# Performance work log

Hardware: AMD Instinct MI355X
Metric: run time of the kernel (lower is better)

## Reference

```python
import jax, jax.numpy as jnp
import numpy as np

N_EMBED = 1024
N_HEAD = 16
HEAD_SIZE = N_EMBED // N_HEAD  # 64
SEQ = 2048
BATCH = 2
EPS = 1e-5


def setup_inputs() -> dict:
    key = jax.random.key(0)
    ks = jax.random.split(key, 16)
    s = lambda fan_in: 1.0 / np.sqrt(fan_in)
    d, h, hs, f = N_EMBED, N_HEAD, HEAD_SIZE, 4 * N_EMBED
    return {
        "x": jax.random.normal(ks[0], (BATCH, SEQ, d), dtype=jnp.float32),
        # per-head QKV projections (no bias), stacked over heads: [H, D, hs]
        "wq": jax.random.normal(ks[1], (h, d, hs), dtype=jnp.float32) * s(d),
        "wk": jax.random.normal(ks[2], (h, d, hs), dtype=jnp.float32) * s(d),
        "wv": jax.random.normal(ks[3], (h, d, hs), dtype=jnp.float32) * s(d),
        "w_proj": jax.random.normal(ks[4], (d, d), dtype=jnp.float32) * s(d),
        "b_proj": jnp.zeros((d,), dtype=jnp.float32),
        "w1": jax.random.normal(ks[5], (d, f), dtype=jnp.float32) * s(d),
        "b1": jnp.zeros((f,), dtype=jnp.float32),
        "w2": jax.random.normal(ks[6], (f, d), dtype=jnp.float32) * s(f),
        "b2": jnp.zeros((d,), dtype=jnp.float32),
        "g1": jnp.ones((d,), dtype=jnp.float32),
        "be1": jnp.zeros((d,), dtype=jnp.float32),
        "g2": jnp.ones((d,), dtype=jnp.float32),
        "be2": jnp.zeros((d,), dtype=jnp.float32),
    }


def _layer_norm(x, gamma, beta):
    mu = jnp.mean(x, axis=-1, keepdims=True)
    var = jnp.mean(jnp.square(x - mu), axis=-1, keepdims=True)
    return (x - mu) * jax.lax.rsqrt(var + EPS) * gamma + beta


def reference(x, wq, wk, wv, w_proj, b_proj, w1, b1, w2, b2, g1, be1, g2, be2):
    B, S, D = x.shape
    # per-head projections (vectorized over heads): [B, H, S, hs]
    q = jnp.einsum("bsd,hdk->bhsk", x, wq)
    k = jnp.einsum("bsd,hdk->bhsk", x, wk)
    v = jnp.einsum("bsd,hdk->bhsk", x, wv)
    scale = HEAD_SIZE ** -0.5
    scores = jnp.einsum("bhsk,bhtk->bhst", q, k) * scale  # [B,H,S,S]
    causal = jnp.tril(jnp.ones((S, S), dtype=bool))
    scores = jnp.where(causal, scores, -jnp.inf)
    w = jax.nn.softmax(scores, axis=-1)  # dropout=0 -> identity
    attn = jnp.einsum("bhst,bhtk->bhsk", w, v)  # [B,H,S,hs]
    # concat heads (head-major ordering matches torch.cat over heads)
    attn = attn.transpose(0, 2, 1, 3).reshape(B, S, D)
    y = attn @ w_proj + b_proj
    x = _layer_norm(x + y, g1, be1)
    y = jax.nn.relu(x @ w1 + b1) @ w2 + b2
    x = _layer_norm(x + y, g2, be2)
    return x
```

## Files before the change

kernel.cpp:

```cpp
#include <hip/hip_runtime.h>


typedef unsigned short u16;
typedef unsigned int u32;
typedef __attribute__((ext_vector_type(8))) short bf16x8;
typedef __attribute__((ext_vector_type(4))) float f32x4;
typedef __attribute__((ext_vector_type(2))) u32 u32x2;
typedef __attribute__((ext_vector_type(4))) _Float16 f16x4;

#define MFMA16(a, b, c) __builtin_amdgcn_mfma_f32_16x16x32_bf16(a, b, c, 0, 0, 0)
#define MFMAH(a, b, c) __builtin_amdgcn_mfma_f32_16x16x16f16(a, b, c, 0, 0, 0)

__device__ __forceinline__ u16 f2b(float f) {
  unsigned int u = __builtin_bit_cast(unsigned int, f);
  u = (u + 0x7fffu + ((u >> 16) & 1u)) >> 16;
  return (u16)u;
}

__device__ __forceinline__ void gload_lds16(const u16* g, u16* l) {
  __builtin_amdgcn_global_load_lds((const __attribute__((address_space(1))) void*)g,
                                   (__attribute__((address_space(3))) void*)l, 16, 0, 0);
}

__device__ __forceinline__ u32 pkrtz(float lo, float hi) {
  return __builtin_bit_cast(u32, __builtin_amdgcn_cvt_pkrtz(lo, hi));
}

__device__ __forceinline__ f16x4 pack4h(float a, float b, float c, float d) {
  u32x2 r = {pkrtz(a, b), pkrtz(c, d)};
  return __builtin_bit_cast(f16x4, r);
}

__device__ __forceinline__ u16 f2h(float v) {
  return __builtin_bit_cast(u16, (_Float16)v);
}


__global__ __launch_bounds__(256) void pack_all(
    const float* __restrict__ x, const float* __restrict__ wq,
    const float* __restrict__ wk, const float* __restrict__ wv,
    const float* __restrict__ wp, const float* __restrict__ w1,
    const float* __restrict__ w2, u16* __restrict__ Xbf, u16* __restrict__ WqkvT,
    u16* __restrict__ WprojT, u16* __restrict__ W1T, u16* __restrict__ W2T) {
  int bid = blockIdx.x;
  int t = threadIdx.x;
  if (bid >= 12288) {
    size_t i = ((size_t)(bid - 12288) * 256 + t) * 4;
    float4 v = *(const float4*)(x + i);
    Xbf[i + 0] = f2b(v.x);
    Xbf[i + 1] = f2b(v.y);
    Xbf[i + 2] = f2b(v.z);
    Xbf[i + 3] = f2b(v.w);
    return;
  }
  __shared__ float tile[32][33];
  int tx = t & 31, ty = t >> 5;
  const float* src;
  u16* dst;
  int R, C, r0, c0;
  float scale = 1.0f;
  if (bid < 3072) {
    int z = bid >> 6, q = bid & 63;
    int p = z >> 4, h = z & 15;
    src = (p == 0 ? wq : (p == 1 ? wk : wv)) + (size_t)h * 1024 * 64;
    scale = (p == 0) ? 0.1803368801f : 1.0f;
    dst = WqkvT + (size_t)(p * 1024 + h * 64) * 1024;
    R = 1024; C = 64;
    c0 = (q & 1) * 32; r0 = (q >> 1) * 32;
  } else if (bid < 4096) {
    int q = bid - 3072;
    src = wp; dst = WprojT; R = 1024; C = 1024;
    c0 = (q & 31) * 32; r0 = (q >> 5) * 32;
  } else if (bid < 8192) {
    int q = bid - 4096;
    src = w1; dst = W1T; R = 1024; C = 4096;
    c0 = (q & 127) * 32; r0 = (q >> 7) * 32;
  } else {
    int q = bid - 8192;
    src = w2; dst = W2T; R = 4096; C = 1024;
    c0 = (q & 31) * 32; r0 = (q >> 5) * 32;
  }
#pragma unroll
  for (int i = 0; i < 4; ++i)
    tile[ty + i * 8][tx] = src[(size_t)(r0 + ty + i * 8) * C + c0 + tx];
  __syncthreads();
#pragma unroll
  for (int i = 0; i < 4; ++i)
    dst[(size_t)(c0 + ty + i * 8) * R + r0 + tx] = f2b(tile[tx][ty + i * 8] * scale);
}


template <int MODE>
__global__ __launch_bounds__(256, 4) void gemm_bf16(const u16* __restrict__ A,
                                                    const u16* __restrict__ Bt, int M,
                                                    int N, int Kc, int lda,
                                                    const float* __restrict__ bias,
                                                    u16* __restrict__ outB, int ldc,
                                                    u16* __restrict__ vtg) {
  constexpr int BM = 128, BN = 128, BK = 64;
  constexpr int IM = 4, JN = 4;
  __shared__ u16 As[BM * BK];
  __shared__ u16 Bs[BN * BK];
  int t = threadIdx.x;
  int m0 = blockIdx.x * BM, n0 = blockIdx.y * BN;
  int kb = blockIdx.z * Kc;
  int lane = t & 63, wid = t >> 6;
  int wm = (wid >> 1) * 64, wn = (wid & 1) * 64;
  int m16 = lane & 15, quad = lane >> 4;
  int sw = m16 & 7;

  f32x4 acc[IM][JN] = {};

  for (int k0 = kb; k0 < kb + Kc; k0 += BK) {
    __syncthreads();
#pragma unroll
    for (int i = 0; i < 4; ++i) {
      int S = i * 256 + t;
      int row = S >> 3, c = S & 7;
      gload_lds16(&A[(size_t)(m0 + row) * lda + k0 + (c ^ (row & 7)) * 8],
                  &As[(i * 256 + wid * 64) * 8]);
    }
#pragma unroll
    for (int i = 0; i < 4; ++i) {
      int S = i * 256 + t;
      int row = S >> 3, c = S & 7;
      gload_lds16(&Bt[(size_t)(n0 + row) * lda + k0 + (c ^ (row & 7)) * 8],
                  &Bs[(i * 256 + wid * 64) * 8]);
    }
    __syncthreads();
#pragma unroll
    for (int kk = 0; kk < 2; ++kk) {
      bf16x8 af[IM], bfr[JN];
      int slot = (kk * 4 + quad) ^ sw;
#pragma unroll
      for (int i = 0; i < IM; ++i)
        af[i] = *(const bf16x8*)&As[(wm + i * 16 + m16) * BK + slot * 8];
#pragma unroll
      for (int j = 0; j < JN; ++j)
        bfr[j] = *(const bf16x8*)&Bs[(wn + j * 16 + m16) * BK + slot * 8];
#pragma unroll
      for (int i = 0; i < IM; ++i)
#pragma unroll
        for (int j = 0; j < JN; ++j) acc[i][j] = MFMA16(af[i], bfr[j], acc[i][j]);
    }
  }

  if (MODE == 3 && n0 >= 2048) {
#pragma unroll
    for (int i = 0; i < IM; ++i)
#pragma unroll
      for (int j = 0; j < JN; ++j) {
        int dg = n0 + wn + j * 16 + m16 - 2048;
        int hh = dg >> 6, dd = dg & 63;
        int token = m0 + wm + i * 16 + quad * 4;
        int bb = token >> 11, tt = token & 2047;
        u32x2 pv = {pkrtz(acc[i][j][0], acc[i][j][1]),
                    pkrtz(acc[i][j][2], acc[i][j][3])};
        *(u32x2*)&vtg[(((size_t)bb * 16 + hh) * 64 + dd) * 2048 + tt] = pv;
      }
    return;
  }

  u16* pb = (MODE == 4) ? outB + (size_t)blockIdx.z * M * N : outB;
#pragma unroll
  for (int i = 0; i < IM; ++i)
#pragma unroll
    for (int j = 0; j < JN; ++j) {
      int col = n0 + wn + j * 16 + m16;
      float bv = (MODE == 1) ? bias[col] : 0.0f;
#pragma unroll
      for (int r = 0; r < 4; ++r) {
        int row = m0 + wm + i * 16 + quad * 4 + r;
        float v = acc[i][j][r];
        if (MODE == 1) {
          v += bv;
          v = v > 0.0f ? v : 0.0f;
          pb[(size_t)row * ldc + col] = f2b(v);
        } else if (MODE == 4) {
          pb[(size_t)row * ldc + col] = f2h(v);
        } else {
          pb[(size_t)row * ldc + col] = f2b(v);
        }
      }
    }
}


__constant__ unsigned char R_QB[40] = {
    15, 15, 15, 15, 14, 14, 11, 11, 11, 10, 7,  7,  3,
    14, 14, 13, 13, 13, 13, 12, 12, 10, 10, 9,  9,  6,  6,
    12, 12, 9,  8,  8,  8,  5,  5,  2,
    4,  4,  1,  0};
__constant__ unsigned char R_K0[40] = {
    0,  8,  16, 24, 0,  8,  0,  8,  16, 0,  0,  8,  0,
    16, 23, 0,  7,  14, 21, 0,  7,  8,  15, 0,  7,  0,  7,
    14, 20, 14, 0,  6,  12, 0,  6,  0,
    0,  5,  0,  0};
__constant__ unsigned char R_NIT[40] = {
    8, 8, 8, 8, 8, 8, 8, 8, 8, 8, 8, 8, 8,
    7, 7, 7, 7, 7, 7, 7, 7, 7, 7, 7, 7, 7, 7,
    6, 6, 6, 6, 6, 6, 6, 6, 6,
    5, 5, 4, 2};
__constant__ unsigned char R_ST[40] = {
    32, 33, 34, 35, 28, 29, 17, 18, 19, 14, 6,  7,  255,
    30, 31, 24, 25, 26, 27, 20, 21, 15, 16, 11, 12, 4,  5,
    22, 23, 13, 8,  9,  10, 2,  3,  255,
    0,  1,  255, 255};
__constant__ unsigned char CB_BASE[12] = {0, 2, 4, 6, 8, 11, 14, 17, 20, 24, 28, 32};

__global__ __launch_bounds__(256) void attn_part(const u16* __restrict__ qk,
                                                 const u16* __restrict__ vtg,
                                                 u16* __restrict__ attn_out,
                                                 u16* __restrict__ opart0,
                                                 u16* __restrict__ opart1,
                                                 float2* __restrict__ ml) {
  int rank = blockIdx.x >> 5, bh = blockIdx.x & 31;
  int qb = R_QB[rank];
  int k_start = R_K0[rank] * 64;
  int iters = R_NIT[rank];
  int st = R_ST[rank];
  int b = bh >> 4, h = bh & 15;

  int t = threadIdx.x, lane = t & 63, w = t >> 6;
  int m16 = lane & 15, quad = lane >> 4;
  int wq0 = qb * 128 + w * 32;

  __shared__ u16 Ks[2][64 * 64];
  __shared__ u16 Vs[2][64 * 64];

  bf16x8 qa[2][2];
#pragma unroll
  for (int qs = 0; qs < 2; ++qs) {
    const u16* qp = qk + (size_t)(b * 2048 + wq0 + qs * 16 + m16) * 2048 + h * 64;
    qa[qs][0] = *(const bf16x8*)&qp[quad * 8];
    qa[qs][1] = *(const bf16x8*)&qp[32 + quad * 8];
  }

  f32x4 oT[2][4] = {};
  f32x4 oL[2] = {};
  const f16x4 ones = {(_Float16)1.0f, (_Float16)1.0f, (_Float16)1.0f, (_Float16)1.0f};

  int row0 = t >> 3, c0 = t & 7;
  int row1 = 32 + row0;
  const u16* kbase = qk + (size_t)(b * 2048) * 2048 + 1024 + h * 64;
  const u16* vbase = vtg + ((size_t)(b * 16 + h) * 64) * 2048;
  int sw = m16 & 7;

#define STAGE_ASYNC(T0, BUF)                                                        \
  {                                                                                 \
    gload_lds16(&kbase[(size_t)((T0) + row0) * 2048 + (c0 ^ (row0 & 7)) * 8],       \
                &Ks[BUF][(w * 64) * 8]);                                            \
    gload_lds16(&kbase[(size_t)((T0) + row1) * 2048 + (c0 ^ (row1 & 7)) * 8],       \
                &Ks[BUF][(256 + w * 64) * 8]);                                      \
    gload_lds16(&vbase[(size_t)row0 * 2048 + (T0) + (c0 ^ (row0 & 7)) * 8],         \
                &Vs[BUF][(w * 64) * 8]);                                            \
    gload_lds16(&vbase[(size_t)row1 * 2048 + (T0) + (c0 ^ (row1 & 7)) * 8],         \
                &Vs[BUF][(256 + w * 64) * 8]);                                      \
  }

  STAGE_ASYNC(k_start, 0);
  __syncthreads();

  for (int it = 0; it < iters; ++it) {
    int t0 = k_start + it * 64;
    int cur = it & 1;
    if (it + 1 < iters) STAGE_ASYNC(t0 + 64, !cur);

    if (t0 <= wq0 + 31) {
      f32x4 sv[2][4];
      __builtin_amdgcn_s_setprio(1);
#pragma unroll
      for (int ts = 0; ts < 4; ++ts) {
        bf16x8 ka0 = *(const bf16x8*)&Ks[cur][(ts * 16 + m16) * 64 + (quad ^ sw) * 8];
        bf16x8 ka1 =
            *(const bf16x8*)&Ks[cur][(ts * 16 + m16) * 64 + ((4 + quad) ^ sw) * 8];
#pragma unroll
        for (int qs = 0; qs < 2; ++qs) {
          f32x4 a = {};
          a = MFMA16(ka0, qa[qs][0], a);
          a = MFMA16(ka1, qa[qs][1], a);
          sv[qs][ts] = a;
        }
      }
      __builtin_amdgcn_s_setprio(0);
      if (t0 + 63 > wq0) {
#pragma unroll
        for (int qs = 0; qs < 2; ++qs)
#pragma unroll
          for (int ts = 0; ts < 4; ++ts)
#pragma unroll
            for (int rr = 0; rr < 4; ++rr) {
              int key = t0 + ts * 16 + quad * 4 + rr;
              if (key > wq0 + qs * 16 + m16) sv[qs][ts][rr] = -3e38f;
            }
      }
      f16x4 pf[2][4];
#pragma unroll
      for (int qs = 0; qs < 2; ++qs)
#pragma unroll
        for (int ts = 0; ts < 4; ++ts) {
          float p0 = exp2f(sv[qs][ts][0] - 8.0f);
          float p1 = exp2f(sv[qs][ts][1] - 8.0f);
          float p2 = exp2f(sv[qs][ts][2] - 8.0f);
          float p3 = exp2f(sv[qs][ts][3] - 8.0f);
          pf[qs][ts] = pack4h(p0, p1, p2, p3);
        }
      __builtin_amdgcn_s_setprio(1);
#pragma unroll
      for (int ts = 0; ts < 4; ++ts) {
        oL[0] = MFMAH(ones, pf[0][ts], oL[0]);
        oL[1] = MFMAH(ones, pf[1][ts], oL[1]);
#pragma unroll
        for (int ds = 0; ds < 4; ++ds) {
          f16x4 av = __builtin_bit_cast(
              f16x4, *(const u32x2*)&Vs[cur][(ds * 16 + m16) * 64 +
                                             (((ts * 2 + (quad >> 1)) ^ sw) * 8) +
                                             (quad & 1) * 4]);
          oT[0][ds] = MFMAH(av, pf[0][ts], oT[0][ds]);
          oT[1][ds] = MFMAH(av, pf[1][ts], oT[1][ds]);
        }
      }
      __builtin_amdgcn_s_setprio(0);
    }
    __syncthreads();
  }
#undef STAGE_ASYNC

  if (st == 255) {
#pragma unroll
    for (int qs = 0; qs < 2; ++qs) {
      float rl = 1.0f / oL[qs][0];
      int q = wq0 + qs * 16 + m16;
#pragma unroll
      for (int ds = 0; ds < 4; ++ds) {
        f32x4 o = oT[qs][ds];
        u32x2 ov = {(u32)f2b(o[0] * rl) | ((u32)f2b(o[1] * rl) << 16),
                    (u32)f2b(o[2] * rl) | ((u32)f2b(o[3] * rl) << 16)};
        *(u32x2*)&attn_out[(size_t)(b * 2048 + q) * 1024 + h * 64 + ds * 16 +
                           quad * 4] = ov;
      }
    }
  } else {
    u16* po;
    size_t sb;
    if (st < 32) {
      po = opart0;
      sb = ((size_t)st * 32 + bh) * 128;
    } else {
      po = opart1;
      sb = ((size_t)(st - 32) * 32 + bh) * 128;
    }
    size_t mlb = ((size_t)st * 32 + bh) * 128;
#pragma unroll
    for (int qs = 0; qs < 2; ++qs) {
      float ls = oL[qs][0];
      int qloc = w * 32 + qs * 16 + m16;
#pragma unroll
      for (int ds = 0; ds < 4; ++ds) {
        f32x4 o = oT[qs][ds];
        u32x2 ov = {pkrtz(o[0], o[1]), pkrtz(o[2], o[3])};
        *(u32x2*)&po[(sb + qloc) * 64 + ds * 16 + quad * 4] = ov;
      }
      if (quad == 0) ml[mlb + qloc] = make_float2(0.0f, ls);
    }
  }
}

__global__ __launch_bounds__(256) void attn_comb(const u16* __restrict__ opart0,
                                                 const u16* __restrict__ opart1,
                                                 const float2* __restrict__ ml,
                                                 u16* __restrict__ attn_out) {
  int qb = 4 + blockIdx.x, bh = blockIdx.y;
  int b = bh >> 4, h = bh & 15;
  int nseg = (qb < 8) ? 2 : (qb < 12 ? 3 : 4);
  int base = CB_BASE[qb - 4];
  int t = threadIdx.x;
  int q = t >> 1, dh = (t & 1) * 32;

  float lsum = 0.0f;
  for (int s = 0; s < nseg; ++s)
    lsum += ml[((size_t)(base + s) * 32 + bh) * 128 + q].y;
  float rl = 1.0f / lsum;

  constexpr size_t SLOT = (size_t)32 * 128 * 64;
  const u16* orow[4];
  for (int s = 0; s < nseg; ++s) {
    int sa = base + s;
    const u16* bp =
        (sa < 32) ? opart0 + (size_t)sa * SLOT : opart1 + (size_t)(sa - 32) * SLOT;
    orow[s] = bp + ((size_t)bh * 128 + q) * 64 + dh;
  }

  size_t oout = (size_t)(b * 2048 + qb * 128 + q) * 1024 + h * 64 + dh;
#pragma unroll 2
  for (int dd = 0; dd < 32; dd += 4) {
    float o0 = 0, o1 = 0, o2 = 0, o3 = 0;
    for (int s = 0; s < nseg; ++s) {
      f16x4 hv = __builtin_bit_cast(f16x4, *(const u32x2*)&orow[s][dd]);
      o0 += (float)hv[0];
      o1 += (float)hv[1];
      o2 += (float)hv[2];
      o3 += (float)hv[3];
    }
    u32x2 ov = {(u32)f2b(o0 * rl) | ((u32)f2b(o1 * rl) << 16),
                (u32)f2b(o2 * rl) | ((u32)f2b(o3 * rl) << 16)};
    *(u32x2*)&attn_out[oout + dd] = ov;
  }
}


__global__ __launch_bounds__(256) void ln_comb(const u16* __restrict__ parts, int np,
                                               const float* __restrict__ bias,
                                               const float* __restrict__ resid,
                                               const float* __restrict__ g,
                                               const float* __restrict__ be,
                                               float* __restrict__ outF,
                                               u16* __restrict__ outB) {
  int row = blockIdx.x;
  int t = threadIdx.x;
  size_t off = (size_t)row * 1024 + t * 4;
  float4 bv4 = *(const float4*)(bias + t * 4);
  float a0 = bv4.x, a1 = bv4.y, a2 = bv4.z, a3 = bv4.w;
  for (int c = 0; c < np; ++c) {
    f16x4 hv =
        __builtin_bit_cast(f16x4, *(const u32x2*)&parts[(size_t)c * 4096 * 1024 + off]);
    a0 += (float)hv[0];
    a1 += (float)hv[1];
    a2 += (float)hv[2];
    a3 += (float)hv[3];
  }
  float4 rv = *(const float4*)(resid + off);
  a0 += rv.x;
  a1 += rv.y;
  a2 += rv.z;
  a3 += rv.w;

  float s = a0 + a1 + a2 + a3;
  float sq = a0 * a0 + a1 * a1 + a2 * a2 + a3 * a3;
#pragma unroll
  for (int d = 1; d < 64; d <<= 1) {
    s += __shfl_xor(s, d);
    sq += __shfl_xor(sq, d);
  }
  __shared__ float red[8];
  int lane = t & 63, wid = t >> 6;
  if (lane == 0) {
    red[wid] = s;
    red[4 + wid] = sq;
  }
  __syncthreads();
  s = red[0] + red[1] + red[2] + red[3];
  sq = red[4] + red[5] + red[6] + red[7];
  float mu = s * (1.0f / 1024.0f);
  float var = sq * (1.0f / 1024.0f) - mu * mu;
  float rstd = rsqrtf(var + 1e-5f);
  float4 gv = *(const float4*)(g + t * 4);
  float4 bev = *(const float4*)(be + t * 4);
  float o0 = (a0 - mu) * rstd * gv.x + bev.x;
  float o1 = (a1 - mu) * rstd * gv.y + bev.y;
  float o2 = (a2 - mu) * rstd * gv.z + bev.z;
  float o3 = (a3 - mu) * rstd * gv.w + bev.w;
  if (outF) {
    float4 ov = {o0, o1, o2, o3};
    *(float4*)(outF + off) = ov;
  }
  if (outB) {
    outB[off + 0] = f2b(o0);
    outB[off + 1] = f2b(o1);
    outB[off + 2] = f2b(o2);
    outB[off + 3] = f2b(o3);
  }
}


extern "C" void kernel_launch(void* const* d_in, const int* in_sizes, int n_in,
                              void* d_out, int out_size, void* d_ws, size_t ws_size,
                              hipStream_t stream) {
  const float* x = (const float*)d_in[0];
  const float* wq = (const float*)d_in[1];
  const float* wk = (const float*)d_in[2];
  const float* wv = (const float*)d_in[3];
  const float* w_proj = (const float*)d_in[4];
  const float* b_proj = (const float*)d_in[5];
  const float* w1 = (const float*)d_in[6];
  const float* b1 = (const float*)d_in[7];
  const float* w2 = (const float*)d_in[8];
  const float* b2 = (const float*)d_in[9];
  const float* g1 = (const float*)d_in[10];
  const float* be1 = (const float*)d_in[11];
  const float* g2 = (const float*)d_in[12];
  const float* be2 = (const float*)d_in[13];
  float* out = (float*)d_out;

  const int M = 4096;
  char* w = (char*)d_ws;
  u16* Xbf = (u16*)w;        w += (size_t)M * 1024 * 2;
  u16* WqkvT = (u16*)w;      w += (size_t)3072 * 1024 * 2;
  u16* WprojT = (u16*)w;     w += (size_t)1024 * 1024 * 2;
  u16* W1T = (u16*)w;        w += (size_t)4096 * 1024 * 2;
  u16* X1b = (u16*)w;        w += (size_t)M * 1024 * 2;
  u16* W2T = (u16*)w;        w += (size_t)1024 * 4096 * 2;
  u16* QK = (u16*)w;         w += (size_t)M * 2048 * 2;
  u16* Vtg = (u16*)w;        w += (size_t)2 * 16 * 64 * 2048 * 2;
  u16* Attn = (u16*)w;       w += (size_t)M * 1024 * 2;
  float* X1f = (float*)w;    w += (size_t)M * 1024 * 4;

  u16* Pdown = Xbf;
  u16* Pproj = QK;
  u16* Hbuf = QK;
  u16* Opart0 = (u16*)X1f;
  u16* Opart1 = Xbf;
  float2* Ml = (float2*)((char*)d_ws + (size_t)4 * 1024 * 1024);

  pack_all<<<16384, 256, 0, stream>>>(x, wq, wk, wv, w_proj, w1, w2, Xbf, WqkvT,
                                      WprojT, W1T, W2T);

  gemm_bf16<3><<<dim3(32, 24, 1), 256, 0, stream>>>(Xbf, WqkvT, M, 3072, 1024, 1024,
                                                    nullptr, QK, 2048, Vtg);

  attn_part<<<1280, 256, 0, stream>>>(QK, Vtg, Attn, Opart0, Opart1, Ml);
  attn_comb<<<dim3(12, 32), 256, 0, stream>>>(Opart0, Opart1, Ml, Attn);

  gemm_bf16<4><<<dim3(32, 8, 2), 256, 0, stream>>>(Attn, WprojT, M, 1024, 512, 1024,
                                                   nullptr, Pproj, 1024, nullptr);
  ln_comb<<<M, 256, 0, stream>>>(Pproj, 2, b_proj, x, g1, be1, X1f, X1b);

  gemm_bf16<1><<<dim3(32, 32, 1), 256, 0, stream>>>(X1b, W1T, M, 4096, 1024, 1024, b1,
                                                    Hbuf, 4096, nullptr);

  gemm_bf16<4><<<dim3(32, 8, 4), 256, 0, stream>>>(Hbuf, W2T, M, 1024, 1024, 4096,
                                                   nullptr, Pdown, 1024, nullptr);
  ln_comb<<<M, 256, 0, stream>>>(Pdown, 4, b2, X1f, g2, be2, out, nullptr);
}
```

Measured before the change: 330.9 us.

## Add 256x256-tile 8-wave GEMM kernel for the FFN up-projection

New measurement: 365.1 us. +10.3%, slower.

```diff
diff --git a/kernel.cpp b/kernel.cpp
--- a/kernel.cpp
+++ b/kernel.cpp
@@ -186,6 +186,180 @@
 }
 
 
+template <int MODE>
+__global__ __launch_bounds__(512) void gemm8(const u16* __restrict__ A,
+                                             const u16* __restrict__ Bt, int M, int N,
+                                             int Kc, int lda,
+                                             const float* __restrict__ bias,
+                                             u16* __restrict__ outB, int ldc) {
+  __shared__ __align__(16) u16 As[2][2][128 * 64];
+  __shared__ __align__(16) u16 Bs[2][2][128 * 64];
+  int t = threadIdx.x;
+  int lane = t & 63, wid = t >> 6;
+  int m16 = lane & 15, quad = lane >> 4, sw = m16 & 7;
+  int wr = wid >> 2, wc = wid & 3;
+  int m0 = blockIdx.x * 256, n0 = blockIdx.y * 256;
+  int kb = blockIdx.z * Kc;
+  int NT = Kc >> 6;
+
+  int ahalf = t >> 8;
+  int at = t & 255;
+  int aw = wid & 3;
+  int brow0 = (wc & 1) * 64;
+
+  f32x4 acc[8][4] = {};
+  bf16x8 afc[2][2], afn[2][2], bfc[4][2], bfn[4][2];
+
+#define STAGE_B(bf, bh, kt)                                                        \
+  {                                                                                \
+    _Pragma("unroll") for (int l = 0; l < 2; ++l) {                                \
+      int slot = l * 512 + t;                                                      \
+      int row = slot >> 3, c = slot & 7;                                           \
+      gload_lds16(&Bt[(size_t)(n0 + (bh)*128 + row) * lda + kb + (kt)*64 +         \
+                      (c ^ (row & 7)) * 8],                                        \
+                  &Bs[bf][bh][(l * 512 + wid * 64) * 8]);                          \
+    }                                                                              \
+  }
+
+#define STAGE_A(bf, qp, kt)                                                        \
+  {                                                                                \
+    _Pragma("unroll") for (int l = 0; l < 2; ++l) {                                \
+      int slot = l * 256 + at;                                                     \
+      int row = slot >> 3, c = slot & 7;                                           \
+      int lrow = (qp)*64 + row;                                                    \
+      gload_lds16(&A[(size_t)(m0 + ahalf * 128 + lrow) * lda + kb + (kt)*64 +      \
+                     (c ^ (row & 7)) * 8],                                         \
+                  &As[bf][ahalf][((qp)*512 + l * 256 + aw * 64) * 8]);             \
+    }                                                                              \
+  }
+
+#define READ_AF(dst, base, qdv)                                                    \
+  {                                                                                \
+    _Pragma("unroll") for (int mi = 0; mi < 2; ++mi)                               \
+        _Pragma("unroll") for (int kk = 0; kk < 2; ++kk)                           \
+            dst[mi][kk] = *(const bf16x8*)&(base)[((qdv)*32 + mi * 16 + m16) * 64 +\
+                                                  ((kk * 4 + quad) ^ sw) * 8];     \
+  }
+
+#define READ_BF(dst, base)                                                         \
+  {                                                                                \
+    _Pragma("unroll") for (int j = 0; j < 4; ++j)                                  \
+        _Pragma("unroll") for (int kk = 0; kk < 2; ++kk)                           \
+            dst[j][kk] = *(const bf16x8*)&(base)[(brow0 + j * 16 + m16) * 64 +     \
+                                                 ((kk * 4 + quad) ^ sw) * 8];      \
+  }
+
+  STAGE_B(0, 0, 0);
+  STAGE_B(0, 1, 0);
+  STAGE_A(0, 0, 0);
+  STAGE_A(0, 1, 0);
+  if (NT > 1) {
+    STAGE_B(1, 0, 1);
+    STAGE_B(1, 1, 1);
+    STAGE_A(1, 0, 1);
+    asm volatile("s_waitcnt vmcnt(6)" ::: "memory");
+  } else {
+    asm volatile("s_waitcnt vmcnt(0)" ::: "memory");
+  }
+  __builtin_amdgcn_s_barrier();
+  asm volatile("" ::: "memory");
+  READ_BF(bfc, &Bs[0][wc >> 1][0]);
+  READ_AF(afc, &As[0][wr][0], 0);
+
+  for (int kt = 0; kt < NT; ++kt) {
+    int buf = kt & 1;
+    const u16* Ab = &As[buf][wr][0];
+    const u16* Abn = &As[buf ^ 1][wr][0];
+    const u16* Bbn = &Bs[buf ^ 1][wc >> 1][0];
+#pragma unroll
+    for (int qd = 0; qd < 4; ++qd) {
+      if (qd < 3) {
+        READ_AF(afn, Ab, qd + 1);
+      } else if (kt + 1 < NT) {
+        READ_BF(bfn, Bbn);
+        READ_AF(afn, Abn, 0);
+      }
+      if (qd == 0) {
+        if (kt + 1 < NT) STAGE_A(buf ^ 1, 1, kt + 1);
+      } else if (qd == 1) {
+        if (kt + 2 < NT) STAGE_B(buf, 0, kt + 2);
+      } else if (qd == 2) {
+        if (kt + 2 < NT) STAGE_B(buf, 1, kt + 2);
+      } else {
+        if (kt + 2 < NT) STAGE_A(buf, 0, kt + 2);
+      }
+      if (qd < 3)
+        asm volatile("s_waitcnt lgkmcnt(4)" ::: "memory");
+      else if (kt + 1 < NT)
+        asm volatile("s_waitcnt lgkmcnt(12)" ::: "memory");
+      else
+        asm volatile("s_waitcnt lgkmcnt(0)" ::: "memory");
+      __builtin_amdgcn_sched_barrier(0);
+      __builtin_amdgcn_s_setprio(1);
+#pragma unroll
+      for (int mi = 0; mi < 2; ++mi)
+#pragma unroll
+        for (int j = 0; j < 4; ++j)
+#pragma unroll
+          for (int kk = 0; kk < 2; ++kk)
+            acc[qd * 2 + mi][j] = MFMA16(afc[mi][kk], bfc[j][kk], acc[qd * 2 + mi][j]);
+      __builtin_amdgcn_s_setprio(0);
+      if (qd == 0) {
+        if (kt + 1 < NT)
+          asm volatile("s_waitcnt vmcnt(8)" ::: "memory");
+        else
+          asm volatile("s_waitcnt vmcnt(0)" ::: "memory");
+      } else if (qd == 2) {
+        if (kt + 2 < NT)
+          asm volatile("s_waitcnt vmcnt(6)" ::: "memory");
+        else
+          asm volatile("s_waitcnt vmcnt(0)" ::: "memory");
+      }
+      if (qd < 3 || kt + 1 < NT) {
+#pragma unroll
+        for (int mi = 0; mi < 2; ++mi)
+#pragma unroll
+          for (int kk = 0; kk < 2; ++kk) afc[mi][kk] = afn[mi][kk];
+        if (qd == 3) {
+#pragma unroll
+          for (int j = 0; j < 4; ++j)
+#pragma unroll
+            for (int kk = 0; kk < 2; ++kk) bfc[j][kk] = bfn[j][kk];
+        }
+      }
+      asm volatile("" ::: "memory");
+      __builtin_amdgcn_s_barrier();
+      asm volatile("" ::: "memory");
+    }
+  }
+
+  u16* pb = (MODE == 4) ? outB + (size_t)blockIdx.z * M * N : outB;
+#pragma unroll
+  for (int mf = 0; mf < 8; ++mf)
+#pragma unroll
+    for (int j = 0; j < 4; ++j) {
+      int col = n0 + wc * 64 + j * 16 + m16;
+      float bv = (MODE == 1) ? bias[col] : 0.0f;
+#pragma unroll
+      for (int r = 0; r < 4; ++r) {
+        int row = m0 + wr * 128 + mf * 16 + quad * 4 + r;
+        float v = acc[mf][j][r];
+        if (MODE == 1) {
+          v += bv;
+          v = v > 0.0f ? v : 0.0f;
+          pb[(size_t)row * ldc + col] = f2b(v);
+        } else {
+          pb[(size_t)row * ldc + col] = f2h(v);
+        }
+      }
+    }
+#undef STAGE_B
+#undef STAGE_A
+#undef READ_AF
+#undef READ_BF
+}
+
+
 __constant__ unsigned char R_QB[40] = {
     15, 15, 15, 15, 14, 14, 11, 11, 11, 10, 7,  7,  3,
     14, 14, 13, 13, 13, 13, 12, 12, 10, 10, 9,  9,  6,  6,
@@ -525,8 +699,8 @@
                                                    nullptr, Pproj, 1024, nullptr);
   ln_comb<<<M, 256, 0, stream>>>(Pproj, 2, b_proj, x, g1, be1, X1f, X1b);
 
-  gemm_bf16<1><<<dim3(32, 32, 1), 256, 0, stream>>>(X1b, W1T, M, 4096, 1024, 1024, b1,
-                                                    Hbuf, 4096, nullptr);
+  gemm8<1><<<dim3(16, 16, 1), 512, 0, stream>>>(X1b, W1T, M, 4096, 1024, 1024, b1,
+                                                Hbuf, 4096);
 
   gemm_bf16<4><<<dim3(32, 8, 4), 256, 0, stream>>>(Hbuf, W2T, M, 1024, 1024, 4096,
                                                    nullptr, Pdown, 1024, nullptr);
```
